# Performance work log

Hardware: AMD Instinct MI355X
Metric: run time of the kernel (lower is better)

The kernel has to match this reference:

```python
import jax, jax.numpy as jnp
import numpy as np

N = 500_000          # total nodes (25000 graphs x 20 joints)
E = 800_000          # total edges (25000 graphs x 32 edges)
NUM_EDGES = 32       # edges per graph (module init arg)
IN_C = 128
OUT_C = 256
LN_EPS = 1e-5


def setup_inputs() -> dict:
    key = jax.random.key(0)
    ks = jax.random.split(key, 8)
    x = jax.random.normal(ks[0], (N, IN_C), dtype=jnp.float32)
    edge_index = jax.random.randint(ks[1], (2, E), 0, N, dtype=jnp.int64)
    # learned per-graph edge weights (init ones in torch; randomized positive here)
    edge_weights = jax.random.uniform(ks[2], (NUM_EDGES,), jnp.float32, 0.5, 1.5)
    W_gcn = jax.random.normal(ks[3], (IN_C, OUT_C), jnp.float32) / np.float32(np.sqrt(IN_C))
    b_gcn = jnp.zeros((OUT_C,), jnp.float32)
    W_res = jax.random.normal(ks[4], (IN_C, OUT_C), jnp.float32) / np.float32(np.sqrt(IN_C))
    b_res = jnp.zeros((OUT_C,), jnp.float32)
    gamma = jnp.ones((OUT_C,), jnp.float32)
    beta = jnp.zeros((OUT_C,), jnp.float32)
    return dict(x=x, edge_weights=edge_weights, W_gcn=W_gcn, b_gcn=b_gcn,
                W_res=W_res, b_res=b_res, gamma=gamma, beta=beta,
                edge_index=edge_index)


def reference(x, edge_weights, W_gcn, b_gcn, W_res, b_res, gamma, beta, edge_index):
    n = x.shape[0]
    e_tot = edge_index.shape[1]
    batch_size = e_tot // NUM_EDGES
    ew = jnp.tile(edge_weights, batch_size)            # repeated per-batch weights [E]
    row, col = edge_index[0], edge_index[1]            # source -> target

    # GCN symmetric normalization with implicit self loops (weight 1)
    deg = jax.ops.segment_sum(ew, col, num_segments=n) + 1.0   # [N]
    dinv = jax.lax.rsqrt(deg)                                   # [N]
    norm = dinv[row] * ew * dinv[col]                           # [E]

    xw = x @ W_gcn                                              # [N, OUT_C]
    agg = jax.ops.segment_sum(norm[:, None] * xw[row], col, num_segments=n)
    # self-loop contribution: norm_ii = dinv_i * 1 * dinv_i = 1/deg_i
    gcn_out = agg + xw * (dinv * dinv)[:, None] + b_gcn         # [N, OUT_C]

    res = x @ W_res + b_res                                     # residual Linear
    h = gcn_out + res

    mu = jnp.mean(h, axis=-1, keepdims=True)
    var = jnp.mean((h - mu) ** 2, axis=-1, keepdims=True)
    hn = (h - mu) * jax.lax.rsqrt(var + LN_EPS)
    return jax.nn.relu(hn * gamma + beta)
```

## Files before the change

kernel.cpp:

```cpp
#include <hip/hip_runtime.h>
#include <hip/hip_bf16.h>

typedef __attribute__((ext_vector_type(8))) short short8;
typedef __attribute__((ext_vector_type(8))) unsigned short ushort8;
typedef __attribute__((ext_vector_type(4))) float f32x4;
typedef unsigned short u16;

#define IN_C 128
#define OUT_C 256
#define LN_EPS 1e-5f

__device__ __forceinline__ u16 f2bf(float f) {
    __hip_bfloat16 h = __float2bfloat16(f);
    return __builtin_bit_cast(u16, h);
}

__global__ void k_count(const int* __restrict__ ei, const float* __restrict__ ew,
                        float* __restrict__ deg, int* __restrict__ cnt, int E, int nbc,
                        const float* __restrict__ Wg, const float* __restrict__ Wr,
                        const float* __restrict__ bg, const float* __restrict__ br,
                        u16* __restrict__ wfrag, float* __restrict__ bc) {
    int b = blockIdx.x;
    if (b < nbc) {
        int e = b * 256 + threadIdx.x;
        if (e < E) {
            int c = ei[E + e];
            atomicAdd(&deg[c], ew[e & 31]);
            atomicAdd(&cnt[c], 1);
        }
        return;
    }
    int tid = (b - nbc) * 256 + threadIdx.x;
    if (tid < OUT_C) bc[tid] = bg[tid] + br[tid];
    if (tid >= 8192) return;
    int l = tid & 63;
    int t = (tid >> 6) & 15;
    int s = tid >> 10;
    int n = t * 16 + (l & 15);
    int k0 = s * 32 + (l >> 4) * 8;
    short8 pk;
#pragma unroll
    for (int j = 0; j < 8; ++j) {
        int k = k0 + j;
        float w = (k < IN_C) ? Wg[k * OUT_C + n] : Wr[(k - IN_C) * OUT_C + n];
        pk[j] = (short)f2bf(w);
    }
    reinterpret_cast<short8*>(wfrag)[tid] = pk;
}

__global__ void k_scan1(const int* __restrict__ cnt, int* __restrict__ partial,
                        float* __restrict__ deg, int n) {
    __shared__ int sm[256];
    int b = blockIdx.x, t = threadIdx.x;
    int base = b * 1024 + t * 4;
    int s = 0;
#pragma unroll
    for (int k = 0; k < 4; ++k) {
        int i = base + k;
        if (i < n) { s += cnt[i]; deg[i] = rsqrtf(1.0f + deg[i]); }
    }
    sm[t] = s; __syncthreads();
    for (int m = 128; m > 0; m >>= 1) { if (t < m) sm[t] += sm[t + m]; __syncthreads(); }
    if (t == 0) partial[b] = sm[0];
}

__global__ void k_scan2(int* __restrict__ partial, int nb) {
    __shared__ int sm[512];
    int t = threadIdx.x;
    sm[t] = (t < nb) ? partial[t] : 0;
    __syncthreads();
    for (int d = 1; d < 512; d <<= 1) {
        int v = (t >= d) ? sm[t - d] : 0;
        __syncthreads();
        sm[t] += v;
        __syncthreads();
    }
    if (t < nb) partial[t] = (t == 0) ? 0 : sm[t - 1];
}

__global__ void k_scan3(const int* __restrict__ cnt, const int* __restrict__ partial,
                        int* __restrict__ off, int* __restrict__ cur, int n, int E) {
    __shared__ int sm[256];
    int b = blockIdx.x, t = threadIdx.x;
    int base = b * 1024 + t * 4;
    int c[4]; int s = 0;
#pragma unroll
    for (int k = 0; k < 4; ++k) { int i = base + k; c[k] = (i < n) ? cnt[i] : 0; s += c[k]; }
    sm[t] = s; __syncthreads();
    for (int d = 1; d < 256; d <<= 1) {
        int v = (t >= d) ? sm[t - d] : 0;
        __syncthreads();
        sm[t] += v;
        __syncthreads();
    }
    int run = partial[b] + (sm[t] - s);
#pragma unroll
    for (int k = 0; k < 4; ++k) {
        int i = base + k;
        if (i < n) { off[i] = run; cur[i] = run; }
        run += c[k];
    }
    if (b == 0 && t == 0) off[n] = E;
}

__global__ void k_place(const int* __restrict__ ei, const float* __restrict__ ew,
                        const float* __restrict__ dinv, int* __restrict__ cur,
                        int2* __restrict__ rec2, int E) {
    int e = blockIdx.x * 256 + threadIdx.x;
    if (e >= E) return;
    int r = ei[e], c = ei[E + e];
    float nrm = dinv[r] * ew[e & 31] * dinv[c];
    int p = atomicAdd(&cur[c], 1);
    rec2[p] = make_int2(r, __float_as_int(nrm));
}

__global__ __launch_bounds__(512, 4) void k_gemm(
    const float4* __restrict__ x4, const float* __restrict__ dinv,
    const int* __restrict__ off, const int2* __restrict__ rec2g,
    const u16* __restrict__ wfrag, const float* __restrict__ bc,
    const float* __restrict__ gamma, const float* __restrict__ beta,
    float* __restrict__ out, int N) {

    __shared__ u16 A[32 * 264];
    __shared__ float red[8 * 32 * 2];
    __shared__ float fin[32 * 2];

    const int tid = threadIdx.x;
    const int lane = tid & 63;
    const int wv = tid >> 6;
    const long r0 = (long)blockIdx.x * 32;

    const int trow = tid >> 4;
    const int tq = tid & 15;
    const long gr = r0 + trow;

    float ua[8];
    int p0 = 0, p1 = 0;
    {
        u16* xp = &A[trow * 264 + 128 + tq * 8];
        if (gr < N) {
            float d = dinv[gr];
            float d2 = d * d;
            const float4* xs = x4 + gr * 32 + tq * 2;
            float4 v0 = xs[0], v1 = xs[1];
            ushort8 xx;
            xx[0] = f2bf(v0.x); xx[1] = f2bf(v0.y); xx[2] = f2bf(v0.z); xx[3] = f2bf(v0.w);
            xx[4] = f2bf(v1.x); xx[5] = f2bf(v1.y); xx[6] = f2bf(v1.z); xx[7] = f2bf(v1.w);
            *reinterpret_cast<ushort8*>(xp) = xx;
            ua[0] = v0.x * d2; ua[1] = v0.y * d2; ua[2] = v0.z * d2; ua[3] = v0.w * d2;
            ua[4] = v1.x * d2; ua[5] = v1.y * d2; ua[6] = v1.z * d2; ua[7] = v1.w * d2;
            p0 = off[gr]; p1 = off[gr + 1];
        } else {
#pragma unroll
            for (int k = 0; k < 8; ++k) ua[k] = 0.f;
            ushort8 zz = {0, 0, 0, 0, 0, 0, 0, 0};
            *reinterpret_cast<ushort8*>(xp) = zz;
        }
    }

    for (int p = p0; p < p1; p += 4) {
        const int nb = p1 - p;
        int sr[4]; float nr[4];
        float4 ga[4][2];
#pragma unroll
        for (int b = 0; b < 4; ++b) {
            if (b < nb) {
                int2 rc = rec2g[p + b];
                sr[b] = rc.x;
                nr[b] = __int_as_float(rc.y);
            }
        }
#pragma unroll
        for (int b = 0; b < 4; ++b) {
            if (b < nb) {
                const float4* xr = x4 + (long)sr[b] * 32 + tq * 2;
                ga[b][0] = xr[0];
                ga[b][1] = xr[1];
            }
        }
#pragma unroll
        for (int b = 0; b < 4; ++b) {
            if (b < nb) {
                ua[0] += nr[b] * ga[b][0].x; ua[1] += nr[b] * ga[b][0].y;
                ua[2] += nr[b] * ga[b][0].z; ua[3] += nr[b] * ga[b][0].w;
                ua[4] += nr[b] * ga[b][1].x; ua[5] += nr[b] * ga[b][1].y;
                ua[6] += nr[b] * ga[b][1].z; ua[7] += nr[b] * ga[b][1].w;
            }
        }
    }

    {
        ushort8 uu;
        uu[0] = f2bf(ua[0]); uu[1] = f2bf(ua[1]); uu[2] = f2bf(ua[2]); uu[3] = f2bf(ua[3]);
        uu[4] = f2bf(ua[4]); uu[5] = f2bf(ua[5]); uu[6] = f2bf(ua[6]); uu[7] = f2bf(ua[7]);
        u16* up = &A[trow * 264 + tq * 8];
        *reinterpret_cast<ushort8*>(up) = uu;
    }
    __syncthreads();

    const short8* wf = reinterpret_cast<const short8*>(wfrag);
    short8 bfr[8][2];
#pragma unroll
    for (int s = 0; s < 8; ++s) {
#pragma unroll
        for (int t = 0; t < 2; ++t)
            bfr[s][t] = wf[(s * 16 + (wv * 2 + t)) * 64 + lane];
    }

    f32x4 acc[2][2];
#pragma unroll
    for (int m = 0; m < 2; ++m)
#pragma unroll
        for (int t = 0; t < 2; ++t) acc[m][t] = (f32x4){0.f, 0.f, 0.f, 0.f};

    const int arowb = lane & 15;
    const int koff = (lane >> 4) * 8;
#pragma unroll
    for (int s = 0; s < 8; ++s) {
#pragma unroll
        for (int m = 0; m < 2; ++m) {
            short8 af = *reinterpret_cast<const short8*>(
                &A[(m * 16 + arowb) * 264 + s * 32 + koff]);
#pragma unroll
            for (int t = 0; t < 2; ++t)
                acc[m][t] = __builtin_amdgcn_mfma_f32_16x16x32_bf16(af, bfr[s][t], acc[m][t], 0, 0, 0);
        }
    }

    const int ncol = lane & 15;
    const int g = lane >> 4;
    const float bc0 = bc[wv * 32 + ncol];
    const float bc1 = bc[wv * 32 + 16 + ncol];
#pragma unroll
    for (int m = 0; m < 2; ++m) {
#pragma unroll
        for (int j = 0; j < 4; ++j) {
            float v0 = acc[m][0][j] + bc0;
            float v1 = acc[m][1][j] + bc1;
            acc[m][0][j] = v0;
            acc[m][1][j] = v1;
            float s = v0 + v1;
            float q = v0 * v0 + v1 * v1;
#pragma unroll
            for (int msk = 1; msk < 16; msk <<= 1) {
                s += __shfl_xor(s, msk);
                q += __shfl_xor(q, msk);
            }
            if (ncol == 0) {
                int row = m * 16 + g * 4 + j;
                red[(wv * 32 + row) * 2 + 0] = s;
                red[(wv * 32 + row) * 2 + 1] = q;
            }
        }
    }
    __syncthreads();
    if (tid < 64) {
        int row = tid >> 1, q = tid & 1;
        float t = 0.f;
#pragma unroll
        for (int w = 0; w < 8; ++w) t += red[(w * 32 + row) * 2 + q];
        fin[row * 2 + q] = t;
    }
    __syncthreads();

    const float gv0 = gamma[wv * 32 + ncol], bv0 = beta[wv * 32 + ncol];
    const float gv1 = gamma[wv * 32 + 16 + ncol], bv1 = beta[wv * 32 + 16 + ncol];
#pragma unroll
    for (int m = 0; m < 2; ++m) {
#pragma unroll
        for (int j = 0; j < 4; ++j) {
            int row = m * 16 + g * 4 + j;
            long rr = r0 + row;
            if (rr < N) {
                float mean = fin[row * 2] * (1.f / 256.f);
                float var = fin[row * 2 + 1] * (1.f / 256.f) - mean * mean;
                float rstd = rsqrtf(var + LN_EPS);
                float o0 = (acc[m][0][j] - mean) * rstd * gv0 + bv0;
                float o1 = (acc[m][1][j] - mean) * rstd * gv1 + bv1;
                float* op = out + rr * (long)OUT_C + wv * 32 + ncol;
                op[0]  = fmaxf(o0, 0.f);
                op[16] = fmaxf(o1, 0.f);
            }
        }
    }
}

extern "C" void kernel_launch(void* const* d_in, const int* in_sizes, int n_in,
                              void* d_out, int out_size, void* d_ws, size_t ws_size,
                              hipStream_t stream) {
    const float* x    = (const float*)d_in[0];
    const float* ew   = (const float*)d_in[1];
    const float* Wg   = (const float*)d_in[2];
    const float* bg   = (const float*)d_in[3];
    const float* Wr   = (const float*)d_in[4];
    const float* br   = (const float*)d_in[5];
    const float* gm   = (const float*)d_in[6];
    const float* bt   = (const float*)d_in[7];
    const int*   ei   = (const int*)d_in[8];

    const int N = in_sizes[0] / IN_C;
    const int E = in_sizes[8] / 2;
    const int NB1 = (N + 1023) / 1024;
    const int NBC = (E + 255) / 256;

    int2*  rec2 = (int2*)d_ws;
    float* deg  = (float*)(rec2 + E);
    int*   cnt  = (int*)(deg + N);
    int*   off  = cnt + N;
    int*   cur  = off + N + 1;
    int*   part = cur + N;
    u16*   wfrag = (u16*)(part + 512);
    float* bc   = (float*)(wfrag + 65536);

    hipMemsetAsync(deg, 0, (size_t)N * sizeof(float), stream);
    hipMemsetAsync(cnt, 0, (size_t)N * sizeof(int), stream);
    k_count<<<NBC + 32, 256, 0, stream>>>(ei, ew, deg, cnt, E, NBC,
                                          Wg, Wr, bg, br, wfrag, bc);
    k_scan1<<<NB1, 256, 0, stream>>>(cnt, part, deg, N);
    k_scan2<<<1, 512, 0, stream>>>(part, NB1);
    k_scan3<<<NB1, 256, 0, stream>>>(cnt, part, off, cur, N, E);
    k_place<<<(E + 255) / 256, 256, 0, stream>>>(ei, ew, deg, cur, rec2, E);
    k_gemm<<<(N + 31) / 32, 512, 0, stream>>>((const float4*)x, deg, off, rec2,
                                              wfrag, bc, gm, bt, (float*)d_out, N);
}
```

Baseline: 462.5 us.

## Split fused gather+GEMM into separate gather and GEMM kernels via bf16 buffer

Moves the per-node neighbor aggregation into its own kernel, `k_gather`, with 256-thread blocks. It writes a packed bf16 row per node (aggregated features plus raw x) to a workspace buffer. A new `k_gemm2` loads those rows into LDS and runs the MFMA GEMM plus LayerNorm epilogue. The aim is to decouple the latency-bound irregular gather from the register-heavy GEMM so each can run at its own occupancy. The cost is an extra round trip of about 256 MB of intermediate data through global memory and an extra launch. It also merges the two adjacent memsets into one.

```diff
diff --git a/kernel.cpp b/kernel.cpp
--- a/kernel.cpp
+++ b/kernel.cpp
@@ -114,50 +114,31 @@
     rec2[p] = make_int2(r, __float_as_int(nrm));
 }
 
-__global__ __launch_bounds__(512, 4) void k_gemm(
+__global__ __launch_bounds__(256) void k_gather(
     const float4* __restrict__ x4, const float* __restrict__ dinv,
     const int* __restrict__ off, const int2* __restrict__ rec2g,
-    const u16* __restrict__ wfrag, const float* __restrict__ bc,
-    const float* __restrict__ gamma, const float* __restrict__ beta,
-    float* __restrict__ out, int N) {
-
-    __shared__ u16 A[32 * 264];
-    __shared__ float red[8 * 32 * 2];
-    __shared__ float fin[32 * 2];
-
+    ushort8* __restrict__ apack8, int N) {
     const int tid = threadIdx.x;
-    const int lane = tid & 63;
-    const int wv = tid >> 6;
-    const long r0 = (long)blockIdx.x * 32;
-
-    const int trow = tid >> 4;
     const int tq = tid & 15;
-    const long gr = r0 + trow;
+    const long row = (long)blockIdx.x * 16 + (tid >> 4);
+    if (row >= N) return;
+
+    float d = dinv[row];
+    float d2 = d * d;
+    const float4* xs = x4 + row * 32 + tq * 2;
+    float4 v0 = xs[0], v1 = xs[1];
+
+    ushort8 xx;
+    xx[0] = f2bf(v0.x); xx[1] = f2bf(v0.y); xx[2] = f2bf(v0.z); xx[3] = f2bf(v0.w);
+    xx[4] = f2bf(v1.x); xx[5] = f2bf(v1.y); xx[6] = f2bf(v1.z); xx[7] = f2bf(v1.w);
+    ushort8* ap = apack8 + row * 32;
+    ap[16 + tq] = xx;
 
     float ua[8];
-    int p0 = 0, p1 = 0;
-    {
-        u16* xp = &A[trow * 264 + 128 + tq * 8];
-        if (gr < N) {
-            float d = dinv[gr];
-            float d2 = d * d;
-            const float4* xs = x4 + gr * 32 + tq * 2;
-            float4 v0 = xs[0], v1 = xs[1];
-            ushort8 xx;
-            xx[0] = f2bf(v0.x); xx[1] = f2bf(v0.y); xx[2] = f2bf(v0.z); xx[3] = f2bf(v0.w);
-            xx[4] = f2bf(v1.x); xx[5] = f2bf(v1.y); xx[6] = f2bf(v1.z); xx[7] = f2bf(v1.w);
-            *reinterpret_cast<ushort8*>(xp) = xx;
-            ua[0] = v0.x * d2; ua[1] = v0.y * d2; ua[2] = v0.z * d2; ua[3] = v0.w * d2;
-            ua[4] = v1.x * d2; ua[5] = v1.y * d2; ua[6] = v1.z * d2; ua[7] = v1.w * d2;
-            p0 = off[gr]; p1 = off[gr + 1];
-        } else {
-#pragma unroll
-            for (int k = 0; k < 8; ++k) ua[k] = 0.f;
-            ushort8 zz = {0, 0, 0, 0, 0, 0, 0, 0};
-            *reinterpret_cast<ushort8*>(xp) = zz;
-        }
-    }
-
+    ua[0] = v0.x * d2; ua[1] = v0.y * d2; ua[2] = v0.z * d2; ua[3] = v0.w * d2;
+    ua[4] = v1.x * d2; ua[5] = v1.y * d2; ua[6] = v1.z * d2; ua[7] = v1.w * d2;
+
+    const int p0 = off[row], p1 = off[row + 1];
     for (int p = p0; p < p1; p += 4) {
         const int nb = p1 - p;
         int sr[4]; float nr[4];
@@ -189,12 +170,33 @@
         }
     }
 
-    {
-        ushort8 uu;
-        uu[0] = f2bf(ua[0]); uu[1] = f2bf(ua[1]); uu[2] = f2bf(ua[2]); uu[3] = f2bf(ua[3]);
-        uu[4] = f2bf(ua[4]); uu[5] = f2bf(ua[5]); uu[6] = f2bf(ua[6]); uu[7] = f2bf(ua[7]);
-        u16* up = &A[trow * 264 + tq * 8];
-        *reinterpret_cast<ushort8*>(up) = uu;
+    ushort8 uu;
+    uu[0] = f2bf(ua[0]); uu[1] = f2bf(ua[1]); uu[2] = f2bf(ua[2]); uu[3] = f2bf(ua[3]);
+    uu[4] = f2bf(ua[4]); uu[5] = f2bf(ua[5]); uu[6] = f2bf(ua[6]); uu[7] = f2bf(ua[7]);
+    ap[tq] = uu;
+}
+
+__global__ __launch_bounds__(512, 4) void k_gemm2(
+    const ushort8* __restrict__ apack8, const u16* __restrict__ wfrag,
+    const float* __restrict__ bc, const float* __restrict__ gamma,
+    const float* __restrict__ beta, float* __restrict__ out, int N) {
+
+    __shared__ u16 A[32 * 264];
+    __shared__ float red[8 * 32 * 2];
+    __shared__ float fin[32 * 2];
+
+    const int tid = threadIdx.x;
+    const int lane = tid & 63;
+    const int wv = tid >> 6;
+    const long r0 = (long)blockIdx.x * 32;
+
+    const long cbase = (long)blockIdx.x * 1024;
+#pragma unroll
+    for (int k = 0; k < 2; ++k) {
+        int ch = tid + k * 512;
+        int row = ch >> 5, cir = ch & 31;
+        ushort8 v = apack8[cbase + ch];
+        *reinterpret_cast<ushort8*>(&A[row * 264 + cir * 8]) = v;
     }
     __syncthreads();
 
@@ -304,7 +306,8 @@
     const int NBC = (E + 255) / 256;
 
     int2*  rec2 = (int2*)d_ws;
-    float* deg  = (float*)(rec2 + E);
+    ushort8* apack8 = (ushort8*)(rec2 + E);
+    float* deg  = (float*)(apack8 + (size_t)N * 32);
     int*   cnt  = (int*)(deg + N);
     int*   off  = cnt + N;
     int*   cur  = off + N + 1;
@@ -312,14 +315,15 @@
     u16*   wfrag = (u16*)(part + 512);
     float* bc   = (float*)(wfrag + 65536);
 
-    hipMemsetAsync(deg, 0, (size_t)N * sizeof(float), stream);
-    hipMemsetAsync(cnt, 0, (size_t)N * sizeof(int), stream);
+    hipMemsetAsync(deg, 0, (size_t)N * 2 * sizeof(float), stream);
     k_count<<<NBC + 32, 256, 0, stream>>>(ei, ew, deg, cnt, E, NBC,
                                           Wg, Wr, bg, br, wfrag, bc);
     k_scan1<<<NB1, 256, 0, stream>>>(cnt, part, deg, N);
     k_scan2<<<1, 512, 0, stream>>>(part, NB1);
     k_scan3<<<NB1, 256, 0, stream>>>(cnt, part, off, cur, N, E);
     k_place<<<(E + 255) / 256, 256, 0, stream>>>(ei, ew, deg, cur, rec2, E);
-    k_gemm<<<(N + 31) / 32, 512, 0, stream>>>((const float4*)x, deg, off, rec2,
-                                              wfrag, bc, gm, bt, (float*)d_out, N);
-}
+    k_gather<<<(N + 15) / 16, 256, 0, stream>>>((const float4*)x, deg, off, rec2,
+                                                apack8, N);
+    k_gemm2<<<(N + 31) / 32, 512, 0, stream>>>(apack8, wfrag, bc, gm, bt,
+                                               (float*)d_out, N);
+}
```

New measurement: 463.7 us. About the same (+0.3%).
